# Optimization experiments

Measured on AMD Instinct MI355X. Metric: run time of the kernel, lower is better.

The kernel has to match this reference:

```python
import jax, jax.numpy as jnp
import numpy as np

B, C_IN, N = 8, 3, 32768
C_OUT, K, E = 128, 4, 4194304
TOTAL = B * N
BN_EPS = 1e-5


def setup_inputs() -> dict:
    key = jax.random.key(0)
    ks = jax.random.split(key, 6)
    return {
        "x": jax.random.normal(ks[0], (B, C_IN, N), dtype=jnp.float32),
        "edge_index": jax.random.randint(ks[1], (2, E), 0, TOTAL, dtype=jnp.int32),
        "edge_weight": jax.random.uniform(ks[2], (E,), dtype=jnp.float32),
        # ChebConv parameters: one (in, out) weight per Chebyshev order, plus bias
        "weight": jax.random.normal(ks[3], (K, C_IN, C_OUT), dtype=jnp.float32) * 0.1,
        "bias": jax.random.normal(ks[4], (C_OUT,), dtype=jnp.float32) * 0.01,
        # BatchNorm1d affine params
        "gamma": jnp.ones((C_OUT,), dtype=jnp.float32),
        "beta": jnp.zeros((C_OUT,), dtype=jnp.float32),
    }


def reference(x, edge_index, edge_weight, weight, bias, gamma, beta):
    b, f, n = x.shape
    total = b * n
    # (B, F, N) -> (B*N, F)
    h = x.transpose(0, 2, 1).reshape(total, f)

    src, dst = edge_index[0], edge_index[1]
    # remove_self_loops: zero self-loop weights (diagonal of scaled Laplacian is 0)
    w = jnp.where(src == dst, 0.0, edge_weight)
    # sym-normalized Laplacian, scaled by 2/lambda_max with lambda_max=2 (PyG default),
    # then self-loops added with -1 cancel the +I diagonal -> L_hat = -D^-1/2 A D^-1/2
    deg = jax.ops.segment_sum(w, src, num_segments=total)
    dis = jnp.where(deg > 0, jax.lax.rsqrt(jnp.maximum(deg, 1e-12)), 0.0)
    norm_w = -dis[src] * w * dis[dst]  # (E,)

    def prop(t):  # y[i] = sum_j L_hat[i, j] t[j]
        return jax.ops.segment_sum(norm_w[:, None] * t[src], dst, num_segments=total)

    # Chebyshev recursion: T0 = x, T1 = L_hat x, T_k = 2 L_hat T_{k-1} - T_{k-2}
    tx0 = h
    out = tx0 @ weight[0]
    tx1 = prop(tx0)
    out = out + tx1 @ weight[1]
    for k in range(2, weight.shape[0]):
        tx2 = 2.0 * prop(tx1) - tx0
        out = out + tx2 @ weight[k]
        tx0, tx1 = tx1, tx2
    out = out + bias

    # BatchNorm1d (training mode: batch stats, biased variance) + ReLU
    mean = out.mean(axis=0)
    var = out.var(axis=0)
    out = (out - mean) * jax.lax.rsqrt(var + BN_EPS) * gamma + beta
    out = jax.nn.relu(out)

    # (B*N, C_OUT) -> (B, C_OUT, N)
    return out.reshape(b, n, -1).transpose(0, 2, 1)
```

## Files before the change

### kernel.cpp

```cpp
#include <hip/hip_runtime.h>
#include <cstdint>

#define B_    8
#define CIN   3
#define NPTS  32768
#define TOT   (B_*NPTS)
#define COUT  128
#define NE    4194304
#define NF    12
#define NMOM  90
#define MSTRIDE 17
#define BN_EPS 1e-5f

#define NBKT  256
#define BKSZ  1024
#define TILE  4096
#define EPT   16


__global__ __launch_bounds__(256) void k_count(const int* __restrict__ src,
                                               const int* __restrict__ dst,
                                               const float* __restrict__ ew,
                                               int* __restrict__ g_hs,
                                               int* __restrict__ g_hd) {
    __shared__ int hs[NBKT], hd[NBKT];
    int t = threadIdx.x;
    if (t < NBKT) { hs[t] = 0; hd[t] = 0; }
    __syncthreads();
    int base = blockIdx.x * 16384 + t;
    for (int k = 0; k < 64; ++k) {
        int e = base + k * 256;
        int s = src[e], d = dst[e];
        float w = ew[e];
        if (s != d && w != 0.0f) {
            atomicAdd(&hs[s >> 10], 1);
            atomicAdd(&hd[d >> 10], 1);
        }
    }
    __syncthreads();
    if (t < NBKT) {
        if (hs[t]) atomicAdd(g_hs + t, hs[t]);
        if (hd[t]) atomicAdd(g_hd + t, hd[t]);
    }
}

__global__ __launch_bounds__(256) void k_scan2(const int* __restrict__ g_hs,
                                               const int* __restrict__ g_hd,
                                               int* __restrict__ off_s,
                                               int* __restrict__ off_d,
                                               int* __restrict__ gp_s,
                                               int* __restrict__ gp_d) {
    int t = threadIdx.x, lane = t & 63, w = t >> 6;
    __shared__ int wt[2][4];
    int v1 = g_hs[t], v2 = g_hd[t];
    int i1 = v1, i2 = v2;
#pragma unroll
    for (int d = 1; d < 64; d <<= 1) {
        int u1 = __shfl_up(i1, d, 64), u2 = __shfl_up(i2, d, 64);
        if (lane >= d) { i1 += u1; i2 += u2; }
    }
    if (lane == 63) { wt[0][w] = i1; wt[1][w] = i2; }
    __syncthreads();
    int p1 = 0, p2 = 0;
#pragma unroll
    for (int k = 0; k < 4; ++k) if (k < w) { p1 += wt[0][k]; p2 += wt[1][k]; }
    int e1 = p1 + i1 - v1, e2 = p2 + i2 - v2;
    off_s[t] = e1; gp_s[t] = e1;
    off_d[t] = e2; gp_d[t] = e2;
    if (t == 255) { off_s[256] = e1 + v1; off_d[256] = e2 + v2; }
}

__global__ __launch_bounds__(256) void k_scatter(const int* __restrict__ src,
                                                 const int* __restrict__ dst,
                                                 const float* __restrict__ ew,
                                                 int* __restrict__ gpos,
                                                 int2* __restrict__ binned,
                                                 int mode) {
    __shared__ int lhist[NBKT], lbase[NBKT], cnt2[NBKT], gbase[NBKT];
    __shared__ int2 sorted[TILE];
    __shared__ unsigned char sbk[TILE];
    __shared__ int wt[4];
    int t = threadIdx.x;
    if (t < NBKT) { lhist[t] = 0; cnt2[t] = 0; }
    __syncthreads();

    int es[EPT], ed[EPT]; float ef[EPT];
    int base = blockIdx.x * TILE + t;
#pragma unroll
    for (int k = 0; k < EPT; ++k) {
        int e = base + k * 256;
        es[k] = src[e]; ed[k] = dst[e]; ef[k] = ew[e];
    }
#pragma unroll
    for (int k = 0; k < EPT; ++k) {
        if (es[k] != ed[k] && ef[k] != 0.0f) {
            int b = (mode ? ed[k] : es[k]) >> 10;
            atomicAdd(&lhist[b], 1);
        }
    }
    __syncthreads();
    {
        int lane = t & 63, wv = t >> 6;
        int v = (t < NBKT) ? lhist[t] : 0;
        int inc = v;
#pragma unroll
        for (int d = 1; d < 64; d <<= 1) {
            int u = __shfl_up(inc, d, 64);
            if (lane >= d) inc += u;
        }
        if (t < NBKT && lane == 63) wt[wv] = inc;
        __syncthreads();
        if (t < NBKT) {
            int pre = 0;
#pragma unroll
            for (int k2 = 0; k2 < 4; ++k2) if (k2 < wv) pre += wt[k2];
            int excl = pre + inc - v;
            lbase[t] = excl;
            gbase[t] = atomicAdd(gpos + t, v);
        }
    }
    __syncthreads();
#pragma unroll
    for (int k = 0; k < EPT; ++k) {
        if (es[k] != ed[k] && ef[k] != 0.0f) {
            int b, w0;
            if (mode) { b = ed[k] >> 10; w0 = es[k] | ((ed[k] & 1023) << 18); }
            else      { b = es[k] >> 10; w0 = es[k] & 1023; }
            int p = atomicAdd(&cnt2[b], 1);
            int idx = lbase[b] + p;
            sorted[idx] = make_int2(w0, __float_as_int(ef[k]));
            sbk[idx] = (unsigned char)b;
        }
    }
    __syncthreads();
    int tot = lbase[NBKT - 1] + lhist[NBKT - 1];
    for (int i = t; i < tot; i += 256) {
        int b = sbk[i];
        binned[(size_t)gbase[b] + (i - lbase[b])] = sorted[i];
    }
}

__global__ __launch_bounds__(512) void k_degdis(const int* __restrict__ off_s,
                                                const int2* __restrict__ binned,
                                                float* __restrict__ dis) {
    __shared__ float acc[BKSZ];
    int t = threadIdx.x, b = blockIdx.x;
    acc[t] = 0.f; acc[t + 512] = 0.f;
    __syncthreads();
    int b0 = off_s[b], b1 = off_s[b + 1];
    for (int i = b0 + t; i < b1; i += 512) {
        int2 r = binned[i];
        atomicAdd(&acc[r.x], __int_as_float(r.y));
    }
    __syncthreads();
#pragma unroll
    for (int j = 0; j < 2; ++j) {
        int i = t + j * 512;
        float v = acc[i];
        dis[b * BKSZ + i] = (v > 0.f) ? rsqrtf(fmaxf(v, 1e-12f)) : 0.f;
    }
}

__global__ __launch_bounds__(512) void k_prop(const int* __restrict__ off_d,
                                              const int2* __restrict__ binned,
                                              const float* __restrict__ dis,
                                              const float* __restrict__ tin,
                                              const float* __restrict__ tprev,
                                              float* __restrict__ tout,
                                              float scale) {
    __shared__ float acc[BKSZ * 3];
    int t = threadIdx.x, b = blockIdx.x;
    for (int i = t; i < BKSZ * 3; i += 512) acc[i] = 0.f;
    __syncthreads();
    int b0 = off_d[b], b1 = off_d[b + 1];
    for (int i = b0 + t; i < b1; i += 512) {
        int2 r = binned[i];
        int s  = r.x & 0x3FFFF;
        int dl = ((unsigned)r.x) >> 18;
        float nw = __int_as_float(r.y) * dis[s];
        const float* ts = tin + (size_t)s * 3;
        atomicAdd(&acc[dl * 3 + 0], nw * ts[0]);
        atomicAdd(&acc[dl * 3 + 1], nw * ts[1]);
        atomicAdd(&acc[dl * 3 + 2], nw * ts[2]);
    }
    __syncthreads();
#pragma unroll
    for (int j = 0; j < 2; ++j) {
        int i = t + j * 512;
        int n = b * BKSZ + i;
        float dn = -dis[n] * scale;
        float r0 = dn * acc[i * 3 + 0];
        float r1 = dn * acc[i * 3 + 1];
        float r2 = dn * acc[i * 3 + 2];
        if (tprev) {
            r0 -= tprev[n * 3 + 0]; r1 -= tprev[n * 3 + 1]; r2 -= tprev[n * 3 + 2];
        }
        tout[n * 3 + 0] = r0; tout[n * 3 + 1] = r1; tout[n * 3 + 2] = r2;
    }
}


__global__ __launch_bounds__(256) void k_tx0(const float* __restrict__ x,
                                             float* __restrict__ tx0) {
    int i = blockIdx.x * 256 + threadIdx.x;
    int b = i >> 15;
    int n = i & (NPTS - 1);
    const float* xb = x + (size_t)b * CIN * NPTS + n;
    tx0[i * 3 + 0] = xb[0];
    tx0[i * 3 + 1] = xb[NPTS];
    tx0[i * 3 + 2] = xb[2 * NPTS];
}

__device__ __forceinline__ void decode_pair(int o, int& A, int& Bb) {
    if (o < 12) { A = o; Bb = 12; return; }
    int p = o - 12, base = 0; A = 0; Bb = 0;
#pragma unroll
    for (int aa = 0; aa < 12; ++aa) {
        int len = 12 - aa;
        bool in = (p >= base) && (p < base + len);
        if (in) { A = aa; Bb = aa + (p - base); }
        base += len;
    }
}

__global__ __launch_bounds__(256) void k_moments(const float* __restrict__ tx0,
                                                 const float* __restrict__ tx1,
                                                 const float* __restrict__ tx2,
                                                 const float* __restrict__ tx3,
                                                 float* __restrict__ mom) {
    __shared__ float L[256 * 13];
    __shared__ float R[4][96];
    const int tid = threadIdx.x, lane = tid & 63, w = tid >> 6;

    int a1, b1, a2 = 12, b2 = 12;
    decode_pair(lane, a1, b1);
    if (lane < 26) decode_pair(64 + lane, a2, b2);

    float acc1 = 0.0f, acc2 = 0.0f;
    const int TPB = (TOT / 256) / 256;
    for (int t = 0; t < TPB; ++t) {
        int node = (blockIdx.x * TPB + t) * 256 + tid;
        __syncthreads();
        float* Ld = &L[tid * 13];
        Ld[0] = tx0[node * 3 + 0]; Ld[1]  = tx0[node * 3 + 1]; Ld[2]  = tx0[node * 3 + 2];
        Ld[3] = tx1[node * 3 + 0]; Ld[4]  = tx1[node * 3 + 1]; Ld[5]  = tx1[node * 3 + 2];
        Ld[6] = tx2[node * 3 + 0]; Ld[7]  = tx2[node * 3 + 1]; Ld[8]  = tx2[node * 3 + 2];
        Ld[9] = tx3[node * 3 + 0]; Ld[10] = tx3[node * 3 + 1]; Ld[11] = tx3[node * 3 + 2];
        Ld[12] = 1.0f;
        __syncthreads();
        const int nb = w * 64;
#pragma unroll 4
        for (int i = 0; i < 64; ++i) {
            const float* Ln = &L[(nb + i) * 13];
            acc1 += Ln[a1] * Ln[b1];
            if (lane < 26) acc2 += Ln[a2] * Ln[b2];
        }
    }
    R[w][lane] = acc1;
    if (lane < 26) R[w][64 + lane] = acc2;
    __syncthreads();
    if (tid < NMOM) {
        float s = R[0][tid] + R[1][tid] + R[2][tid] + R[3][tid];
        atomicAdd(mom + tid * MSTRIDE, s);
    }
}

__global__ __launch_bounds__(128) void k_prep(const float* __restrict__ mom,
                                              const float* __restrict__ weight,
                                              const float* __restrict__ bias,
                                              const float* __restrict__ gamma,
                                              const float* __restrict__ beta,
                                              float* __restrict__ wp,
                                              float* __restrict__ bp) {
    int c = threadIdx.x;
    float w[NF];
#pragma unroll
    for (int f = 0; f < NF; ++f) w[f] = weight[f * COUT + c];

    const float inv = 1.0f / (float)TOT;
    float mu[NF];
#pragma unroll
    for (int a = 0; a < NF; ++a) mu[a] = mom[a * MSTRIDE] * inv;
    float mw = 0.0f;
#pragma unroll
    for (int a = 0; a < NF; ++a) mw += mu[a] * w[a];

    float q = 0.0f;
    int idx = NF;
#pragma unroll
    for (int a = 0; a < NF; ++a) {
#pragma unroll
        for (int b = a; b < NF; ++b) {
            float S2 = mom[idx++ * MSTRIDE] * inv;
            q += ((a == b) ? 1.0f : 2.0f) * w[a] * w[b] * S2;
        }
    }
    float bc   = bias[c];
    float mean = mw + bc;
    float var  = q - mw * mw;
    float sc   = gamma[c] * rsqrtf(var + BN_EPS);
    float sh   = (bc - mean) * sc + beta[c];
#pragma unroll
    for (int f = 0; f < NF; ++f) wp[f * COUT + c] = w[f] * sc;
    bp[c] = sh;
}

__global__ __launch_bounds__(256) void k_out(const float* __restrict__ tx0,
                                             const float* __restrict__ tx1,
                                             const float* __restrict__ tx2,
                                             const float* __restrict__ tx3,
                                             const float* __restrict__ wp,
                                             const float* __restrict__ bp,
                                             float* __restrict__ out) {
    __shared__ float sw[NF * COUT];
    __shared__ float sb[COUT];
    for (int j = threadIdx.x; j < NF * COUT; j += 256) sw[j] = wp[j];
    if (threadIdx.x < COUT) sb[threadIdx.x] = bp[threadIdx.x];
    __syncthreads();

    int i = blockIdx.x * 256 + threadIdx.x;
    int b = i >> 15;
    int n = i & (NPTS - 1);

    float t[NF];
    t[0] = tx0[i * 3 + 0]; t[1]  = tx0[i * 3 + 1]; t[2]  = tx0[i * 3 + 2];
    t[3] = tx1[i * 3 + 0]; t[4]  = tx1[i * 3 + 1]; t[5]  = tx1[i * 3 + 2];
    t[6] = tx2[i * 3 + 0]; t[7]  = tx2[i * 3 + 1]; t[8]  = tx2[i * 3 + 2];
    t[9] = tx3[i * 3 + 0]; t[10] = tx3[i * 3 + 1]; t[11] = tx3[i * 3 + 2];

    float* o = out + (size_t)b * COUT * NPTS + n;
#pragma unroll 4
    for (int c = 0; c < COUT; ++c) {
        float acc = sb[c];
#pragma unroll
        for (int f = 0; f < NF; ++f) acc += t[f] * sw[f * COUT + c];
        o[(size_t)c * NPTS] = fmaxf(acc, 0.0f);
    }
}


__global__ __launch_bounds__(256) void k_deg_fb(const int* src, const int* dst,
                                                const float* ew, float* deg) {
    int e = blockIdx.x * 256 + threadIdx.x;
    int s = src[e], d = dst[e];
    float w = ew[e];
    if (s != d && w != 0.0f) atomicAdd(deg + s, w);
}
__global__ __launch_bounds__(256) void k_dis_fb(float* deg) {
    int i = blockIdx.x * 256 + threadIdx.x;
    float v = deg[i];
    deg[i] = (v > 0.0f) ? rsqrtf(fmaxf(v, 1e-12f)) : 0.0f;
}
__global__ __launch_bounds__(256) void k_prop_fb(const int* src, const int* dst,
                                                 const float* ew, const float* dis,
                                                 const float* tin, float* tout, float scale) {
    int e = blockIdx.x * 256 + threadIdx.x;
    int s = src[e], d = dst[e];
    if (s == d) return;
    float w = ew[e];
    float nw = -dis[s] * w * dis[d] * scale;
    if (nw == 0.0f) return;
    const float* t = tin + (size_t)s * 3;
    atomicAdd(tout + (size_t)d * 3 + 0, nw * t[0]);
    atomicAdd(tout + (size_t)d * 3 + 1, nw * t[1]);
    atomicAdd(tout + (size_t)d * 3 + 2, nw * t[2]);
}
__global__ __launch_bounds__(256) void k_sub_fb(float* tout, const float* tprev) {
    int i = blockIdx.x * 256 + threadIdx.x;
    tout[i] -= tprev[i];
}


extern "C" void kernel_launch(void* const* d_in, const int* in_sizes, int n_in,
                              void* d_out, int out_size, void* d_ws, size_t ws_size,
                              hipStream_t stream) {
    const float* x      = (const float*)d_in[0];
    const int*   ei     = (const int*)d_in[1];
    const float* ew     = (const float*)d_in[2];
    const float* weight = (const float*)d_in[3];
    const float* bias   = (const float*)d_in[4];
    const float* gamma  = (const float*)d_in[5];
    const float* beta   = (const float*)d_in[6];
    float* out = (float*)d_out;

    const int* src = ei;
    const int* dst = ei + NE;

    dim3 blk(256);
    dim3 gT(TOT / 256);

    const size_t need = ((size_t)2 * NE + (size_t)13 * TOT + 2048 + 1026 + 512 + 1664) * 4;

    if (ws_size >= need) {
        int*   wsI    = (int*)d_ws;
        int2*  binned = (int2*)wsI;
        float* dis    = (float*)(wsI + (size_t)2 * NE);
        float* tx0    = dis + TOT;
        float* tx1    = tx0 + (size_t)3 * TOT;
        float* tx2    = tx1 + (size_t)3 * TOT;
        float* tx3    = tx2 + (size_t)3 * TOT;
        int*   hist_s = (int*)(tx3 + (size_t)3 * TOT);
        int*   hist_d = hist_s + 256;
        float* mom    = (float*)(hist_d + 256);
        int*   off_s  = (int*)(mom + 1536);
        int*   off_d  = off_s + 257;
        int*   gp_s   = off_d + 257;
        int*   gp_d   = gp_s + 256;
        float* wp     = (float*)(gp_d + 256);
        float* bp     = wp + 1536;

        hipMemsetAsync(hist_s, 0, 2048 * sizeof(int), stream);

        k_count  <<<dim3(256),  blk, 0, stream>>>(src, dst, ew, hist_s, hist_d);
        k_scan2  <<<dim3(1),    blk, 0, stream>>>(hist_s, hist_d, off_s, off_d, gp_s, gp_d);
        k_scatter<<<dim3(1024), blk, 0, stream>>>(src, dst, ew, gp_s, binned, 0);
        k_degdis <<<dim3(256),  dim3(512), 0, stream>>>(off_s, binned, dis);
        k_tx0    <<<gT,         blk, 0, stream>>>(x, tx0);
        k_scatter<<<dim3(1024), blk, 0, stream>>>(src, dst, ew, gp_d, binned, 1);

        k_prop<<<dim3(256), dim3(512), 0, stream>>>(off_d, binned, dis, tx0, nullptr, tx1, 1.0f);
        k_prop<<<dim3(256), dim3(512), 0, stream>>>(off_d, binned, dis, tx1, tx0,     tx2, 2.0f);
        k_prop<<<dim3(256), dim3(512), 0, stream>>>(off_d, binned, dis, tx2, tx1,     tx3, 2.0f);

        k_moments<<<dim3(256), blk, 0, stream>>>(tx0, tx1, tx2, tx3, mom);
        k_prep   <<<dim3(1), dim3(128), 0, stream>>>(mom, weight, bias, gamma, beta, wp, bp);
        k_out    <<<gT, blk, 0, stream>>>(tx0, tx1, tx2, tx3, wp, bp, out);
    } else {
        dim3 gE(NE / 256);
        dim3 g3T(3 * TOT / 256);
        float* ws  = (float*)d_ws;
        float* deg = ws;
        float* tx1 = ws + (size_t)TOT;
        float* tx2 = ws + (size_t)4 * TOT;
        float* tx3 = ws + (size_t)7 * TOT;
        float* mom = ws + (size_t)10 * TOT;
        float* wp  = mom + 1536;
        float* bp  = wp + 1536;
        float* tx0 = bp + 128;

        hipMemsetAsync(ws, 0, ((size_t)10 * TOT + 1536) * sizeof(float), stream);

        k_deg_fb<<<gE, blk, 0, stream>>>(src, dst, ew, deg);
        k_dis_fb<<<gT, blk, 0, stream>>>(deg);
        k_tx0   <<<gT, blk, 0, stream>>>(x, tx0);

        k_prop_fb<<<gE, blk, 0, stream>>>(src, dst, ew, deg, tx0, tx1, 1.0f);
        k_prop_fb<<<gE, blk, 0, stream>>>(src, dst, ew, deg, tx1, tx2, 2.0f);
        k_sub_fb <<<g3T, blk, 0, stream>>>(tx2, tx0);
        k_prop_fb<<<gE, blk, 0, stream>>>(src, dst, ew, deg, tx2, tx3, 2.0f);
        k_sub_fb <<<g3T, blk, 0, stream>>>(tx3, tx1);

        k_moments<<<dim3(256), blk, 0, stream>>>(tx0, tx1, tx2, tx3, mom);
        k_prep   <<<dim3(1), dim3(128), 0, stream>>>(mom, weight, bias, gamma, beta, wp, bp);
        k_out    <<<gT, blk, 0, stream>>>(tx0, tx1, tx2, tx3, wp, bp, out);
    }
}
```

Before: 392.3 us.

## Fold edge normalization into binned weights and replace global atomics with partials

```diff
diff --git a/kernel.cpp b/kernel.cpp
--- a/kernel.cpp
+++ b/kernel.cpp
@@ -9,7 +9,6 @@
 #define NE    4194304
 #define NF    12
 #define NMOM  90
-#define MSTRIDE 17
 #define BN_EPS 1e-5f
 
 #define NBKT  256
@@ -21,11 +20,11 @@
 __global__ __launch_bounds__(256) void k_count(const int* __restrict__ src,
                                                const int* __restrict__ dst,
                                                const float* __restrict__ ew,
-                                               int* __restrict__ g_hs,
-                                               int* __restrict__ g_hd) {
+                                               int* __restrict__ hsrow,
+                                               int* __restrict__ hdrow) {
     __shared__ int hs[NBKT], hd[NBKT];
     int t = threadIdx.x;
-    if (t < NBKT) { hs[t] = 0; hd[t] = 0; }
+    hs[t] = 0; hd[t] = 0;
     __syncthreads();
     int base = blockIdx.x * 16384 + t;
     for (int k = 0; k < 64; ++k) {
@@ -38,21 +37,23 @@
         }
     }
     __syncthreads();
-    if (t < NBKT) {
-        if (hs[t]) atomicAdd(g_hs + t, hs[t]);
-        if (hd[t]) atomicAdd(g_hd + t, hd[t]);
-    }
-}
-
-__global__ __launch_bounds__(256) void k_scan2(const int* __restrict__ g_hs,
-                                               const int* __restrict__ g_hd,
+    hsrow[blockIdx.x * NBKT + t] = hs[t];
+    hdrow[blockIdx.x * NBKT + t] = hd[t];
+}
+
+__global__ __launch_bounds__(256) void k_scan2(const int* __restrict__ hsrow,
+                                               const int* __restrict__ hdrow,
                                                int* __restrict__ off_s,
                                                int* __restrict__ off_d,
                                                int* __restrict__ gp_s,
                                                int* __restrict__ gp_d) {
     int t = threadIdx.x, lane = t & 63, w = t >> 6;
     __shared__ int wt[2][4];
-    int v1 = g_hs[t], v2 = g_hd[t];
+    int v1 = 0, v2 = 0;
+    for (int b = 0; b < 256; ++b) {
+        v1 += hsrow[b * NBKT + t];
+        v2 += hdrow[b * NBKT + t];
+    }
     int i1 = v1, i2 = v2;
 #pragma unroll
     for (int d = 1; d < 64; d <<= 1) {
@@ -73,6 +74,7 @@
 __global__ __launch_bounds__(256) void k_scatter(const int* __restrict__ src,
                                                  const int* __restrict__ dst,
                                                  const float* __restrict__ ew,
+                                                 const float* __restrict__ dis,
                                                  int* __restrict__ gpos,
                                                  int2* __restrict__ binned,
                                                  int mode) {
@@ -81,7 +83,7 @@
     __shared__ unsigned char sbk[TILE];
     __shared__ int wt[4];
     int t = threadIdx.x;
-    if (t < NBKT) { lhist[t] = 0; cnt2[t] = 0; }
+    lhist[t] = 0; cnt2[t] = 0;
     __syncthreads();
 
     int es[EPT], ed[EPT]; float ef[EPT];
@@ -101,34 +103,38 @@
     __syncthreads();
     {
         int lane = t & 63, wv = t >> 6;
-        int v = (t < NBKT) ? lhist[t] : 0;
+        int v = lhist[t];
         int inc = v;
 #pragma unroll
         for (int d = 1; d < 64; d <<= 1) {
             int u = __shfl_up(inc, d, 64);
             if (lane >= d) inc += u;
         }
-        if (t < NBKT && lane == 63) wt[wv] = inc;
+        if (lane == 63) wt[wv] = inc;
         __syncthreads();
-        if (t < NBKT) {
-            int pre = 0;
-#pragma unroll
-            for (int k2 = 0; k2 < 4; ++k2) if (k2 < wv) pre += wt[k2];
-            int excl = pre + inc - v;
-            lbase[t] = excl;
-            gbase[t] = atomicAdd(gpos + t, v);
-        }
+        int pre = 0;
+#pragma unroll
+        for (int k2 = 0; k2 < 4; ++k2) if (k2 < wv) pre += wt[k2];
+        lbase[t] = pre + inc - v;
+        gbase[t] = atomicAdd(gpos + t, v);
     }
     __syncthreads();
 #pragma unroll
     for (int k = 0; k < EPT; ++k) {
         if (es[k] != ed[k] && ef[k] != 0.0f) {
-            int b, w0;
-            if (mode) { b = ed[k] >> 10; w0 = es[k] | ((ed[k] & 1023) << 18); }
-            else      { b = es[k] >> 10; w0 = es[k] & 1023; }
+            int b, w0; float wv;
+            if (mode) {
+                b  = ed[k] >> 10;
+                w0 = es[k] | ((ed[k] & 1023) << 18);
+                wv = -ef[k] * dis[es[k]] * dis[ed[k]];
+            } else {
+                b  = es[k] >> 10;
+                w0 = es[k] & 1023;
+                wv = ef[k];
+            }
             int p = atomicAdd(&cnt2[b], 1);
             int idx = lbase[b] + p;
-            sorted[idx] = make_int2(w0, __float_as_int(ef[k]));
+            sorted[idx] = make_int2(w0, __float_as_int(wv));
             sbk[idx] = (unsigned char)b;
         }
     }
@@ -140,63 +146,53 @@
     }
 }
 
-__global__ __launch_bounds__(512) void k_degdis(const int* __restrict__ off_s,
-                                                const int2* __restrict__ binned,
-                                                float* __restrict__ dis) {
+__global__ __launch_bounds__(1024) void k_degdis(const int* __restrict__ off_s,
+                                                 const int2* __restrict__ binned,
+                                                 float* __restrict__ dis) {
     __shared__ float acc[BKSZ];
     int t = threadIdx.x, b = blockIdx.x;
-    acc[t] = 0.f; acc[t + 512] = 0.f;
+    acc[t] = 0.f;
     __syncthreads();
     int b0 = off_s[b], b1 = off_s[b + 1];
-    for (int i = b0 + t; i < b1; i += 512) {
+    for (int i = b0 + t; i < b1; i += 1024) {
         int2 r = binned[i];
         atomicAdd(&acc[r.x], __int_as_float(r.y));
     }
     __syncthreads();
-#pragma unroll
-    for (int j = 0; j < 2; ++j) {
-        int i = t + j * 512;
-        float v = acc[i];
-        dis[b * BKSZ + i] = (v > 0.f) ? rsqrtf(fmaxf(v, 1e-12f)) : 0.f;
-    }
-}
-
-__global__ __launch_bounds__(512) void k_prop(const int* __restrict__ off_d,
-                                              const int2* __restrict__ binned,
-                                              const float* __restrict__ dis,
-                                              const float* __restrict__ tin,
-                                              const float* __restrict__ tprev,
-                                              float* __restrict__ tout,
-                                              float scale) {
+    float v = acc[t];
+    dis[b * BKSZ + t] = (v > 0.f) ? rsqrtf(fmaxf(v, 1e-12f)) : 0.f;
+}
+
+__global__ __launch_bounds__(1024) void k_prop(const int* __restrict__ off_d,
+                                               const int2* __restrict__ binned,
+                                               const float* __restrict__ tin,
+                                               const float* __restrict__ tprev,
+                                               float* __restrict__ tout,
+                                               float scale) {
     __shared__ float acc[BKSZ * 3];
     int t = threadIdx.x, b = blockIdx.x;
-    for (int i = t; i < BKSZ * 3; i += 512) acc[i] = 0.f;
+    for (int i = t; i < BKSZ * 3; i += 1024) acc[i] = 0.f;
     __syncthreads();
     int b0 = off_d[b], b1 = off_d[b + 1];
-    for (int i = b0 + t; i < b1; i += 512) {
+    for (int i = b0 + t; i < b1; i += 1024) {
         int2 r = binned[i];
         int s  = r.x & 0x3FFFF;
         int dl = ((unsigned)r.x) >> 18;
-        float nw = __int_as_float(r.y) * dis[s];
+        float nw = __int_as_float(r.y);
         const float* ts = tin + (size_t)s * 3;
         atomicAdd(&acc[dl * 3 + 0], nw * ts[0]);
         atomicAdd(&acc[dl * 3 + 1], nw * ts[1]);
         atomicAdd(&acc[dl * 3 + 2], nw * ts[2]);
     }
     __syncthreads();
-#pragma unroll
-    for (int j = 0; j < 2; ++j) {
-        int i = t + j * 512;
-        int n = b * BKSZ + i;
-        float dn = -dis[n] * scale;
-        float r0 = dn * acc[i * 3 + 0];
-        float r1 = dn * acc[i * 3 + 1];
-        float r2 = dn * acc[i * 3 + 2];
-        if (tprev) {
-            r0 -= tprev[n * 3 + 0]; r1 -= tprev[n * 3 + 1]; r2 -= tprev[n * 3 + 2];
-        }
-        tout[n * 3 + 0] = r0; tout[n * 3 + 1] = r1; tout[n * 3 + 2] = r2;
-    }
+    int n = b * BKSZ + t;
+    float r0 = scale * acc[t * 3 + 0];
+    float r1 = scale * acc[t * 3 + 1];
+    float r2 = scale * acc[t * 3 + 2];
+    if (tprev) {
+        r0 -= tprev[n * 3 + 0]; r1 -= tprev[n * 3 + 1]; r2 -= tprev[n * 3 + 2];
+    }
+    tout[n * 3 + 0] = r0; tout[n * 3 + 1] = r1; tout[n * 3 + 2] = r2;
 }
 
 
@@ -260,8 +256,7 @@
     if (lane < 26) R[w][64 + lane] = acc2;
     __syncthreads();
     if (tid < NMOM) {
-        float s = R[0][tid] + R[1][tid] + R[2][tid] + R[3][tid];
-        atomicAdd(mom + tid * MSTRIDE, s);
+        mom[blockIdx.x * 96 + tid] = R[0][tid] + R[1][tid] + R[2][tid] + R[3][tid];
     }
 }
 
@@ -272,18 +267,23 @@
                                               const float* __restrict__ beta,
                                               float* __restrict__ wp,
                                               float* __restrict__ bp) {
+    __shared__ float sm[NMOM];
     int c = threadIdx.x;
+    if (c < NMOM) {
+        float s = 0.f;
+        for (int b = 0; b < 256; ++b) s += mom[b * 96 + c];
+        sm[c] = s;
+    }
+    __syncthreads();
+
     float w[NF];
 #pragma unroll
     for (int f = 0; f < NF; ++f) w[f] = weight[f * COUT + c];
 
     const float inv = 1.0f / (float)TOT;
-    float mu[NF];
-#pragma unroll
-    for (int a = 0; a < NF; ++a) mu[a] = mom[a * MSTRIDE] * inv;
     float mw = 0.0f;
 #pragma unroll
-    for (int a = 0; a < NF; ++a) mw += mu[a] * w[a];
+    for (int a = 0; a < NF; ++a) mw += (sm[a] * inv) * w[a];
 
     float q = 0.0f;
     int idx = NF;
@@ -291,7 +291,7 @@
     for (int a = 0; a < NF; ++a) {
 #pragma unroll
         for (int b = a; b < NF; ++b) {
-            float S2 = mom[idx++ * MSTRIDE] * inv;
+            float S2 = sm[idx++] * inv;
             q += ((a == b) ? 1.0f : 2.0f) * w[a] * w[b] * S2;
         }
     }
@@ -389,7 +389,7 @@
     dim3 blk(256);
     dim3 gT(TOT / 256);
 
-    const size_t need = ((size_t)2 * NE + (size_t)13 * TOT + 2048 + 1026 + 512 + 1664) * 4;
+    const size_t need = ((size_t)2 * NE + (size_t)13 * TOT + 131072 + 24576 + 1026 + 512 + 1664) * 4;
 
     if (ws_size >= need) {
         int*   wsI    = (int*)d_ws;
@@ -399,28 +399,26 @@
         float* tx1    = tx0 + (size_t)3 * TOT;
         float* tx2    = tx1 + (size_t)3 * TOT;
         float* tx3    = tx2 + (size_t)3 * TOT;
-        int*   hist_s = (int*)(tx3 + (size_t)3 * TOT);
-        int*   hist_d = hist_s + 256;
-        float* mom    = (float*)(hist_d + 256);
-        int*   off_s  = (int*)(mom + 1536);
+        int*   hsrow  = (int*)(tx3 + (size_t)3 * TOT);
+        int*   hdrow  = hsrow + 65536;
+        float* mom    = (float*)(hdrow + 65536);
+        int*   off_s  = (int*)(mom + 24576);
         int*   off_d  = off_s + 257;
         int*   gp_s   = off_d + 257;
         int*   gp_d   = gp_s + 256;
         float* wp     = (float*)(gp_d + 256);
         float* bp     = wp + 1536;
 
-        hipMemsetAsync(hist_s, 0, 2048 * sizeof(int), stream);
-
-        k_count  <<<dim3(256),  blk, 0, stream>>>(src, dst, ew, hist_s, hist_d);
-        k_scan2  <<<dim3(1),    blk, 0, stream>>>(hist_s, hist_d, off_s, off_d, gp_s, gp_d);
-        k_scatter<<<dim3(1024), blk, 0, stream>>>(src, dst, ew, gp_s, binned, 0);
-        k_degdis <<<dim3(256),  dim3(512), 0, stream>>>(off_s, binned, dis);
+        k_count  <<<dim3(256),  blk, 0, stream>>>(src, dst, ew, hsrow, hdrow);
+        k_scan2  <<<dim3(1),    blk, 0, stream>>>(hsrow, hdrow, off_s, off_d, gp_s, gp_d);
+        k_scatter<<<dim3(1024), blk, 0, stream>>>(src, dst, ew, dis, gp_s, binned, 0);
+        k_degdis <<<dim3(256),  dim3(1024), 0, stream>>>(off_s, binned, dis);
         k_tx0    <<<gT,         blk, 0, stream>>>(x, tx0);
-        k_scatter<<<dim3(1024), blk, 0, stream>>>(src, dst, ew, gp_d, binned, 1);
-
-        k_prop<<<dim3(256), dim3(512), 0, stream>>>(off_d, binned, dis, tx0, nullptr, tx1, 1.0f);
-        k_prop<<<dim3(256), dim3(512), 0, stream>>>(off_d, binned, dis, tx1, tx0,     tx2, 2.0f);
-        k_prop<<<dim3(256), dim3(512), 0, stream>>>(off_d, binned, dis, tx2, tx1,     tx3, 2.0f);
+        k_scatter<<<dim3(1024), blk, 0, stream>>>(src, dst, ew, dis, gp_d, binned, 1);
+
+        k_prop<<<dim3(256), dim3(1024), 0, stream>>>(off_d, binned, tx0, nullptr, tx1, 1.0f);
+        k_prop<<<dim3(256), dim3(1024), 0, stream>>>(off_d, binned, tx1, tx0,     tx2, 2.0f);
+        k_prop<<<dim3(256), dim3(1024), 0, stream>>>(off_d, binned, tx2, tx1,     tx3, 2.0f);
 
         k_moments<<<dim3(256), blk, 0, stream>>>(tx0, tx1, tx2, tx3, mom);
         k_prep   <<<dim3(1), dim3(128), 0, stream>>>(mom, weight, bias, gamma, beta, wp, bp);
@@ -434,11 +432,11 @@
         float* tx2 = ws + (size_t)4 * TOT;
         float* tx3 = ws + (size_t)7 * TOT;
         float* mom = ws + (size_t)10 * TOT;
-        float* wp  = mom + 1536;
+        float* wp  = mom + 24576;
         float* bp  = wp + 1536;
         float* tx0 = bp + 128;
 
-        hipMemsetAsync(ws, 0, ((size_t)10 * TOT + 1536) * sizeof(float), stream);
+        (void)hipMemsetAsync(ws, 0, ((size_t)10 * TOT) * sizeof(float), stream);
 
         k_deg_fb<<<gE, blk, 0, stream>>>(src, dst, ew, deg);
         k_dis_fb<<<gT, blk, 0, stream>>>(deg);
```

Measured after the change: 425.1 us. 1.08x slower.
